# Performance work log

Hardware: AMD Instinct MI355X
Metric: run time of the kernel (lower is better)

The kernel has to match this reference:

```python
import jax, jax.numpy as jnp
import numpy as np

N_NODES = 100000
N_EDGES = 1200000
D_IN = 64
D_OUT = 64


def setup_inputs() -> dict:
    key = jax.random.key(0)
    ks = jax.random.split(key, 8)
    feat = jax.random.normal(ks[0], (N_NODES, D_IN), dtype=jnp.float32)
    src = jax.random.randint(ks[1], (N_EDGES,), 0, N_NODES, dtype=jnp.int32)
    dst = jax.random.randint(ks[2], (N_EDGES,), 0, N_NODES, dtype=jnp.int32)
    edge_weight = jax.random.uniform(ks[3], (N_EDGES, 1), dtype=jnp.float32)
    edge_mask = jax.random.uniform(ks[4], (N_EDGES, 1), dtype=jnp.float32)
    W_self = jax.random.normal(ks[5], (D_OUT, D_IN), dtype=jnp.float32) * (1.0 / np.sqrt(D_IN))
    b_self = jnp.zeros((D_OUT,), dtype=jnp.float32)
    W_neigh = jax.random.normal(ks[6], (D_OUT, D_IN), dtype=jnp.float32) * (1.0 / np.sqrt(D_IN))
    b_neigh = jnp.zeros((D_OUT,), dtype=jnp.float32)
    return {"feat": feat, "src": src, "dst": dst, "edge_weight": edge_weight,
            "edge_mask": edge_mask, "W_self": W_self, "b_self": b_self,
            "W_neigh": W_neigh, "b_neigh": b_neigh}


def reference(feat, src, dst, edge_weight, edge_mask, W_self, b_self, W_neigh, b_neigh):
    # message: gather src feats, scale by per-edge weight and mask  -> [E, D_IN]
    msg = feat[src] * edge_weight * edge_mask
    # mean scatter-reduce over incoming edges per dst node
    neigh_sum = jax.ops.segment_sum(msg, dst, num_segments=N_NODES)  # [N, D_IN]
    deg = jax.ops.segment_sum(jnp.ones((msg.shape[0],), dtype=feat.dtype), dst,
                              num_segments=N_NODES)  # [N]
    h_neigh = neigh_sum / jnp.maximum(deg, 1.0)[:, None]  # zero-degree nodes -> 0 (DGL mean semantics)
    # dual linear fuse
    rst = (feat @ W_self.T + b_self) + (h_neigh @ W_neigh.T + b_neigh)
    return rst
```

## Files before the change

### kernel.cpp

```cpp
#include <hip/hip_runtime.h>

#define NB_MAX   1568
#define CAP      1024
#define BT_EDGES 4096
#define BT_TPB   512
#define EPE      8

typedef __attribute__((ext_vector_type(4))) float floatx4;
typedef __attribute__((ext_vector_type(2))) float floatx2;
typedef __attribute__((ext_vector_type(8))) short bf16x8;

__device__ __forceinline__ unsigned short f32_to_bf16(float f) {
  unsigned u = __float_as_uint(f);
  u = (u + 0x7fffu + ((u >> 16) & 1u)) >> 16;
  return (unsigned short)u;
}
__device__ __forceinline__ unsigned pack2(float a, float b) {
  return (unsigned)f32_to_bf16(a) | ((unsigned)f32_to_bf16(b) << 16);
}
__device__ __forceinline__ bf16x8 zero_bf16x8() {
  bf16x8 v;
#pragma unroll
  for (int i = 0; i < 8; ++i) v[i] = 0;
  return v;
}

#if __has_builtin(__builtin_amdgcn_cvt_pk_fp8_f32)
__device__ __forceinline__ unsigned pack_fp8x4(float a, float b, float c, float d) {
  unsigned v = (unsigned)__builtin_amdgcn_cvt_pk_fp8_f32(a, b, 0, false);
  v = (unsigned)__builtin_amdgcn_cvt_pk_fp8_f32(c, d, (int)v, true);
  return v;
}
#else
__device__ __forceinline__ unsigned sw_f32_fp8(float f) {
  unsigned u = __float_as_uint(f);
  unsigned s = (u >> 24) & 0x80u;
  unsigned au = u & 0x7fffffffu;
  if (au > 0x43E00000u) au = 0x43E00000u;
  au += 0x7FFFFu + ((au >> 20) & 1u);
  int e = (int)(au >> 23) - 120;
  if (e <= 0) return s;
  return s | ((unsigned)e << 3) | ((au >> 20) & 7u);
}
__device__ __forceinline__ unsigned pack_fp8x4(float a, float b, float c, float d) {
  return sw_f32_fp8(a) | (sw_f32_fp8(b) << 8) | (sw_f32_fp8(c) << 16) |
         (sw_f32_fp8(d) << 24);
}
#endif

#if __has_builtin(__builtin_amdgcn_cvt_pk_f32_fp8)
__device__ __forceinline__ void dec4(float* acc, unsigned w32, float wt) {
  floatx2 f0 = __builtin_amdgcn_cvt_pk_f32_fp8((int)w32, false);
  floatx2 f1 = __builtin_amdgcn_cvt_pk_f32_fp8((int)w32, true);
  acc[0] += wt * f0.x; acc[1] += wt * f0.y;
  acc[2] += wt * f1.x; acc[3] += wt * f1.y;
}
#else
__device__ __forceinline__ float sw_fp8_f32(unsigned b) {
  unsigned s = (b & 0x80u) << 24;
  unsigned e = (b >> 3) & 0xFu;
  unsigned m = b & 7u;
  float fn = __uint_as_float(s | ((e + 120u) << 23) | (m << 20));
  float fd = (float)(int)m * 0.001953125f;
  fd = (b & 0x80u) ? -fd : fd;
  return e ? fn : fd;
}
__device__ __forceinline__ void dec4(float* acc, unsigned w32, float wt) {
  acc[0] += wt * sw_fp8_f32(w32 & 0xFF);
  acc[1] += wt * sw_fp8_f32((w32 >> 8) & 0xFF);
  acc[2] += wt * sw_fp8_f32((w32 >> 16) & 0xFF);
  acc[3] += wt * sw_fp8_f32(w32 >> 24);
}
#endif

__global__ __launch_bounds__(BT_TPB) void k_build(
    const float* __restrict__ feat, const int* __restrict__ src,
    const int* __restrict__ dst, const float* __restrict__ ew,
    const float* __restrict__ em, const float* __restrict__ Ws,
    const float* __restrict__ Wn, int* __restrict__ gCursor,
    unsigned* __restrict__ recs, unsigned short* __restrict__ featb,
    unsigned char* __restrict__ featq, unsigned short* __restrict__ Wb,
    int E, int nChunks, int nB) {
  __shared__ unsigned stage[BT_EDGES];
  __shared__ int A[NB_MAX];
  __shared__ int B[NB_MAX];
  __shared__ int waveSums[8];

  const int t = threadIdx.x;
  const int lane = t & 63;
  const int wvid = t >> 6;
  const int e0 = blockIdx.x * BT_EDGES;
  const int eEnd = min(e0 + BT_EDGES, E);
  const int nLocal = eEnd - e0;

  for (int i = t; i < NB_MAX; i += BT_TPB) B[i] = 0;
  __syncthreads();

  int dreg[EPE];
#pragma unroll
  for (int k = 0; k < EPE; ++k) {
    int i = e0 + k * BT_TPB + t;
    dreg[k] = -1;
    if (i < eEnd) {
      int d = dst[i];
      dreg[k] = d;
      atomicAdd(&B[d >> 6], 1);
    }
  }
  __syncthreads();

  {
    const int EPT = 4;
    int b0 = t * EPT;
    int v[EPT];
    int sum = 0;
#pragma unroll
    for (int j = 0; j < EPT; ++j) {
      v[j] = (b0 + j < nB) ? B[b0 + j] : 0;
      sum += v[j];
    }
    int x = sum;
#pragma unroll
    for (int d = 1; d < 64; d <<= 1) {
      int y = __shfl_up(x, d, 64);
      if (lane >= d) x += y;
    }
    if (lane == 63) waveSums[wvid] = x;
    __syncthreads();
    int wprefix = 0;
    for (int i = 0; i < wvid; ++i) wprefix += waveSums[i];
    int run = wprefix + x - sum;
#pragma unroll
    for (int j = 0; j < EPT; ++j) {
      if (b0 + j < nB) A[b0 + j] = run;
      run += v[j];
    }
  }
  __syncthreads();

  for (int i = t; i < nB; i += BT_TPB) {
    int c = B[i];
    int l = A[i];
    int g = c ? atomicAdd(&gCursor[i], c) : 0;
    A[i] = i * CAP + g - l;
    B[i] = l;
  }
  __syncthreads();

#pragma unroll
  for (int k = 0; k < EPE; ++k) {
    int i = e0 + k * BT_TPB + t;
    if (i < eEnd) {
      int d = dreg[k];
      int r = atomicAdd(&B[d >> 6], 1);
      float w = ew[i] * em[i];
      int wq = (int)(w * 511.0f + 0.5f);
      if (wq > 511) wq = 511;
      stage[r] = (unsigned)src[i] | ((unsigned)(d & 63) << 17) |
                 ((unsigned)wq << 23);
    }
  }
  __syncthreads();

  for (int i = t; i < nLocal; i += BT_TPB) {
    int lo = 0, hi = nB;
    while (lo < hi) {
      int mid = (lo + hi) >> 1;
      if (B[mid] > i) hi = mid; else lo = mid + 1;
    }
    int pos = A[lo] + i;
    if (pos < (lo + 1) * CAP)
      recs[pos] = stage[i];
  }

  for (int c = blockIdx.x * BT_TPB + t; c < nChunks; c += gridDim.x * BT_TPB) {
    const float4* fp = reinterpret_cast<const float4*>(feat) + (size_t)c * 2;
    float4 a = fp[0], b = fp[1];
    uint4 o;
    o.x = pack2(a.x, a.y);
    o.y = pack2(a.z, a.w);
    o.z = pack2(b.x, b.y);
    o.w = pack2(b.z, b.w);
    reinterpret_cast<uint4*>(featb)[c] = o;
    uint2 q8;
    q8.x = pack_fp8x4(a.x, a.y, a.z, a.w);
    q8.y = pack_fp8x4(b.x, b.y, b.z, b.w);
    reinterpret_cast<uint2*>(featq)[c] = q8;
  }

  if (blockIdx.x == 0) {
    for (int i = t; i < 1024; i += BT_TPB) {
      int j = i >> 4, c4 = i & 15;
      float4 w4 = reinterpret_cast<const float4*>(Ws)[i];
      float4 n4 = reinterpret_cast<const float4*>(Wn)[i];
      *reinterpret_cast<uint2*>(&Wb[j * 128 + c4 * 4]) =
          make_uint2(pack2(w4.x, w4.y), pack2(w4.z, w4.w));
      *reinterpret_cast<uint2*>(&Wb[j * 128 + 64 + c4 * 4]) =
          make_uint2(pack2(n4.x, n4.y), pack2(n4.z, n4.w));
    }
  }
}

__global__ __launch_bounds__(256) void sage_gather_gemm(
    const unsigned short* __restrict__ featb,
    const unsigned char* __restrict__ featq,
    const unsigned short* __restrict__ Wb, const int* __restrict__ gCursor,
    const unsigned* __restrict__ recs, const float* __restrict__ bs,
    const float* __restrict__ bn, float* __restrict__ out, int N) {
  __shared__ unsigned short An[64][72];
  __shared__ unsigned rawL[CAP];
  __shared__ unsigned srtL[CAP];
  __shared__ int cntS[64], offS[64], curS[64];

  const int t = threadIdx.x;
  const int b = blockIdx.x;
  const int n0 = b * 64;
  const int base = b * CAP;
  const int cb = min(gCursor[b], CAP);

  for (int i = t; i < cb; i += 256) rawL[i] = recs[base + i];
  if (t < 64) cntS[t] = 0;
  __syncthreads();

  for (int i = t; i < cb; i += 256)
    atomicAdd(&cntS[(rawL[i] >> 17) & 63], 1);
  __syncthreads();

  if (t < 64) {
    int c = cntS[t];
    int x = c;
#pragma unroll
    for (int d = 1; d < 64; d <<= 1) {
      int y = __shfl_up(x, d, 64);
      if (t >= d) x += y;
    }
    offS[t] = x - c;
    curS[t] = x - c;
  }
  __syncthreads();

  for (int i = t; i < cb; i += 256) {
    unsigned r = rawL[i];
    int p = atomicAdd(&curS[(r >> 17) & 63], 1);
    srtL[p] = r;
  }
  __syncthreads();

  {
    int nl = t >> 2, q = t & 3;
    int deg = cntS[nl], off = offS[nl];
    float acc[16];
#pragma unroll
    for (int i = 0; i < 16; ++i) acc[i] = 0.f;
    const uint4* fq = reinterpret_cast<const uint4*>(featq);

    uint4 uC, uN;
    float wC = 0.f, wN = 0.f;
    if (deg > 0) {
      unsigned r0 = srtL[off];
      uC = fq[(size_t)(r0 & 0x1FFFF) * 4 + q];
      wC = (float)(r0 >> 23) * (1.0f / 511.0f);
    }
    if (deg > 1) {
      unsigned r1 = srtL[off + 1];
      uN = fq[(size_t)(r1 & 0x1FFFF) * 4 + q];
      wN = (float)(r1 >> 23) * (1.0f / 511.0f);
    }
    for (int j = 0; j < deg; ++j) {
      uint4 u = uC;
      float w = wC;
      uC = uN; wC = wN;
      if (j + 2 < deg) {
        unsigned rn = srtL[off + j + 2];
        uN = fq[(size_t)(rn & 0x1FFFF) * 4 + q];
        wN = (float)(rn >> 23) * (1.0f / 511.0f);
      }
      dec4(acc + 0, u.x, w);
      dec4(acc + 4, u.y, w);
      dec4(acc + 8, u.z, w);
      dec4(acc + 12, u.w, w);
    }
    float inv = 1.0f / fmaxf((float)deg, 1.0f);
    uint4 o0, o1;
    o0.x = pack2(acc[0] * inv, acc[1] * inv);
    o0.y = pack2(acc[2] * inv, acc[3] * inv);
    o0.z = pack2(acc[4] * inv, acc[5] * inv);
    o0.w = pack2(acc[6] * inv, acc[7] * inv);
    o1.x = pack2(acc[8] * inv, acc[9] * inv);
    o1.y = pack2(acc[10] * inv, acc[11] * inv);
    o1.z = pack2(acc[12] * inv, acc[13] * inv);
    o1.w = pack2(acc[14] * inv, acc[15] * inv);
    *reinterpret_cast<uint4*>(&An[nl][q * 16]) = o0;
    *reinterpret_cast<uint4*>(&An[nl][q * 16 + 8]) = o1;
  }
  __syncthreads();

  const int wv = t >> 6;
  const int ln = t & 63;
  const int col = ln & 15;
  const int quad = ln >> 4;
  const int gn = n0 + wv * 16 + col;

  floatx4 acc4[4];
#pragma unroll
  for (int jt = 0; jt < 4; ++jt) {
    float bb = bs[jt * 16 + col] + bn[jt * 16 + col];
    acc4[jt] = (floatx4){bb, bb, bb, bb};
  }

#pragma unroll
  for (int kk = 0; kk < 4; ++kk) {
    bf16x8 af;
    if (kk < 2) {
      if (gn < N) {
        af = *reinterpret_cast<const bf16x8*>(featb + (size_t)gn * 64 + kk * 32 + quad * 8);
      } else {
        af = zero_bf16x8();
      }
    } else {
      af = *reinterpret_cast<const bf16x8*>(&An[wv * 16 + col][(kk - 2) * 32 + quad * 8]);
    }
#pragma unroll
    for (int jt = 0; jt < 4; ++jt) {
      bf16x8 bf = *reinterpret_cast<const bf16x8*>(
          Wb + (jt * 16 + col) * 128 + kk * 32 + quad * 8);
      acc4[jt] = __builtin_amdgcn_mfma_f32_16x16x32_bf16(af, bf, acc4[jt], 0, 0, 0);
    }
  }

#pragma unroll
  for (int jt = 0; jt < 4; ++jt) {
#pragma unroll
    for (int r = 0; r < 4; ++r) {
      int m = quad * 4 + r;
      int g = n0 + wv * 16 + m;
      if (g < N) out[(size_t)g * 64 + jt * 16 + col] = acc4[jt][r];
    }
  }
}

extern "C" void kernel_launch(void* const* d_in, const int* in_sizes, int n_in,
                              void* d_out, int out_size, void* d_ws, size_t ws_size,
                              hipStream_t stream) {
  const float* feat = (const float*)d_in[0];
  const int*   src  = (const int*)d_in[1];
  const int*   dst  = (const int*)d_in[2];
  const float* ew   = (const float*)d_in[3];
  const float* em   = (const float*)d_in[4];
  const float* Ws   = (const float*)d_in[5];
  const float* bs   = (const float*)d_in[6];
  const float* Wn   = (const float*)d_in[7];
  const float* bn   = (const float*)d_in[8];
  float* out = (float*)d_out;

  const int N = in_sizes[0] / 64;
  const int E = in_sizes[1];
  const int nB = (N + 63) / 64;

  unsigned short* featb = (unsigned short*)d_ws;
  unsigned char*  featq = (unsigned char*)(featb + (size_t)N * 64);
  unsigned short* Wb    = (unsigned short*)(featq + (size_t)N * 64);
  unsigned* recs   = (unsigned*)(Wb + 64 * 128);
  int*      gCursor = (int*)(recs + (size_t)NB_MAX * CAP);

  hipMemsetAsync(gCursor, 0, NB_MAX * sizeof(int), stream);

  int nChunks = N * 8;
  int gB = (E + BT_EDGES - 1) / BT_EDGES;

  k_build<<<gB, BT_TPB, 0, stream>>>(feat, src, dst, ew, em, Ws, Wn,
                                     gCursor, recs, featb, featq, Wb,
                                     E, nChunks, nB);
  sage_gather_gemm<<<nB, 256, 0, stream>>>(featb, featq, Wb, gCursor, recs,
                                           bs, bn, out, N);
}
```

Measured before the change: 163.8 us.

## Split per-node edge gather across two thread groups with 512-thread blocks

Doubles the gather/GEMM block to 512 threads. Each destination node's incoming edges are now split by parity between two 4-thread groups, and the partial sums are combined through a new shared-memory buffer before bf16 packing. The MFMA stage is split so that each of 8 waves computes half the output columns. This aims to shorten the serial per-node gather chain and raise memory-level parallelism, at the cost of more shared memory (an extra 16KB), an extra barrier, and possibly lower occupancy.

```diff
diff --git a/kernel.cpp b/kernel.cpp
--- a/kernel.cpp
+++ b/kernel.cpp
@@ -201,7 +201,7 @@
   }
 }
 
-__global__ __launch_bounds__(256) void sage_gather_gemm(
+__global__ __launch_bounds__(512) void sage_gather_gemm(
     const unsigned short* __restrict__ featb,
     const unsigned char* __restrict__ featq,
     const unsigned short* __restrict__ Wb, const int* __restrict__ gCursor,
@@ -210,6 +210,7 @@
   __shared__ unsigned short An[64][72];
   __shared__ unsigned rawL[CAP];
   __shared__ unsigned srtL[CAP];
+  __shared__ float pf[64][64];
   __shared__ int cntS[64], offS[64], curS[64];
 
   const int t = threadIdx.x;
@@ -218,11 +219,11 @@
   const int base = b * CAP;
   const int cb = min(gCursor[b], CAP);
 
-  for (int i = t; i < cb; i += 256) rawL[i] = recs[base + i];
+  for (int i = t; i < cb; i += 512) rawL[i] = recs[base + i];
   if (t < 64) cntS[t] = 0;
   __syncthreads();
 
-  for (int i = t; i < cb; i += 256)
+  for (int i = t; i < cb; i += 512)
     atomicAdd(&cntS[(rawL[i] >> 17) & 63], 1);
   __syncthreads();
 
@@ -239,7 +240,7 @@
   }
   __syncthreads();
 
-  for (int i = t; i < cb; i += 256) {
+  for (int i = t; i < cb; i += 512) {
     unsigned r = rawL[i];
     int p = atomicAdd(&curS[(r >> 17) & 63], 1);
     srtL[p] = r;
@@ -247,8 +248,11 @@
   __syncthreads();
 
   {
-    int nl = t >> 2, q = t & 3;
-    int deg = cntS[nl], off = offS[nl];
+    const int nl = t >> 3;
+    const int g  = (t >> 2) & 1;
+    const int q  = t & 3;
+    const int deg = cntS[nl], off = offS[nl];
+    const int myN = (deg - g + 1) >> 1;
     float acc[16];
 #pragma unroll
     for (int i = 0; i < 16; ++i) acc[i] = 0.f;
@@ -256,22 +260,22 @@
 
     uint4 uC, uN;
     float wC = 0.f, wN = 0.f;
-    if (deg > 0) {
-      unsigned r0 = srtL[off];
+    if (myN > 0) {
+      unsigned r0 = srtL[off + g];
       uC = fq[(size_t)(r0 & 0x1FFFF) * 4 + q];
       wC = (float)(r0 >> 23) * (1.0f / 511.0f);
     }
-    if (deg > 1) {
-      unsigned r1 = srtL[off + 1];
+    if (myN > 1) {
+      unsigned r1 = srtL[off + g + 2];
       uN = fq[(size_t)(r1 & 0x1FFFF) * 4 + q];
       wN = (float)(r1 >> 23) * (1.0f / 511.0f);
     }
-    for (int j = 0; j < deg; ++j) {
+    for (int m = 0; m < myN; ++m) {
       uint4 u = uC;
       float w = wC;
       uC = uN; wC = wN;
-      if (j + 2 < deg) {
-        unsigned rn = srtL[off + j + 2];
+      if (m + 2 < myN) {
+        unsigned rn = srtL[off + g + 2 * (m + 2)];
         uN = fq[(size_t)(rn & 0x1FFFF) * 4 + q];
         wN = (float)(rn >> 23) * (1.0f / 511.0f);
       }
@@ -280,32 +284,45 @@
       dec4(acc + 8, u.z, w);
       dec4(acc + 12, u.w, w);
     }
-    float inv = 1.0f / fmaxf((float)deg, 1.0f);
-    uint4 o0, o1;
-    o0.x = pack2(acc[0] * inv, acc[1] * inv);
-    o0.y = pack2(acc[2] * inv, acc[3] * inv);
-    o0.z = pack2(acc[4] * inv, acc[5] * inv);
-    o0.w = pack2(acc[6] * inv, acc[7] * inv);
-    o1.x = pack2(acc[8] * inv, acc[9] * inv);
-    o1.y = pack2(acc[10] * inv, acc[11] * inv);
-    o1.z = pack2(acc[12] * inv, acc[13] * inv);
-    o1.w = pack2(acc[14] * inv, acc[15] * inv);
-    *reinterpret_cast<uint4*>(&An[nl][q * 16]) = o0;
-    *reinterpret_cast<uint4*>(&An[nl][q * 16 + 8]) = o1;
-  }
-  __syncthreads();
-
-  const int wv = t >> 6;
+
+    if (g == 1) {
+#pragma unroll
+      for (int i = 0; i < 16; ++i) pf[nl][q * 16 + i] = acc[i];
+    }
+    __syncthreads();
+    if (g == 0) {
+      float inv = 1.0f / fmaxf((float)deg, 1.0f);
+#pragma unroll
+      for (int i = 0; i < 16; ++i) acc[i] = (acc[i] + pf[nl][q * 16 + i]) * inv;
+      uint4 o0, o1;
+      o0.x = pack2(acc[0], acc[1]);
+      o0.y = pack2(acc[2], acc[3]);
+      o0.z = pack2(acc[4], acc[5]);
+      o0.w = pack2(acc[6], acc[7]);
+      o1.x = pack2(acc[8], acc[9]);
+      o1.y = pack2(acc[10], acc[11]);
+      o1.z = pack2(acc[12], acc[13]);
+      o1.w = pack2(acc[14], acc[15]);
+      *reinterpret_cast<uint4*>(&An[nl][q * 16]) = o0;
+      *reinterpret_cast<uint4*>(&An[nl][q * 16 + 8]) = o1;
+    }
+  }
+  __syncthreads();
+
+  const int wv8 = t >> 6;
+  const int nt = wv8 & 3;
+  const int jh = wv8 >> 2;
   const int ln = t & 63;
   const int col = ln & 15;
   const int quad = ln >> 4;
-  const int gn = n0 + wv * 16 + col;
-
-  floatx4 acc4[4];
-#pragma unroll
-  for (int jt = 0; jt < 4; ++jt) {
+  const int gn = n0 + nt * 16 + col;
+
+  floatx4 acc4[2];
+#pragma unroll
+  for (int jj = 0; jj < 2; ++jj) {
+    int jt = jh * 2 + jj;
     float bb = bs[jt * 16 + col] + bn[jt * 16 + col];
-    acc4[jt] = (floatx4){bb, bb, bb, bb};
+    acc4[jj] = (floatx4){bb, bb, bb, bb};
   }
 
 #pragma unroll
@@ -318,23 +335,25 @@
         af = zero_bf16x8();
       }
     } else {
-      af = *reinterpret_cast<const bf16x8*>(&An[wv * 16 + col][(kk - 2) * 32 + quad * 8]);
-    }
-#pragma unroll
-    for (int jt = 0; jt < 4; ++jt) {
+      af = *reinterpret_cast<const bf16x8*>(&An[nt * 16 + col][(kk - 2) * 32 + quad * 8]);
+    }
+#pragma unroll
+    for (int jj = 0; jj < 2; ++jj) {
+      int jt = jh * 2 + jj;
       bf16x8 bf = *reinterpret_cast<const bf16x8*>(
           Wb + (jt * 16 + col) * 128 + kk * 32 + quad * 8);
-      acc4[jt] = __builtin_amdgcn_mfma_f32_16x16x32_bf16(af, bf, acc4[jt], 0, 0, 0);
-    }
-  }
-
-#pragma unroll
-  for (int jt = 0; jt < 4; ++jt) {
+      acc4[jj] = __builtin_amdgcn_mfma_f32_16x16x32_bf16(af, bf, acc4[jj], 0, 0, 0);
+    }
+  }
+
+#pragma unroll
+  for (int jj = 0; jj < 2; ++jj) {
+    int jt = jh * 2 + jj;
 #pragma unroll
     for (int r = 0; r < 4; ++r) {
       int m = quad * 4 + r;
-      int g = n0 + wv * 16 + m;
-      if (g < N) out[(size_t)g * 64 + jt * 16 + col] = acc4[jt][r];
+      int g2 = n0 + nt * 16 + m;
+      if (g2 < N) out[(size_t)g2 * 64 + jt * 16 + col] = acc4[jj][r];
     }
   }
 }
@@ -371,6 +390,6 @@
   k_build<<<gB, BT_TPB, 0, stream>>>(feat, src, dst, ew, em, Ws, Wn,
                                      gCursor, recs, featb, featq, Wb,
                                      E, nChunks, nB);
-  sage_gather_gemm<<<nB, 256, 0, stream>>>(featb, featq, Wb, gCursor, recs,
+  sage_gather_gemm<<<nB, 512, 0, stream>>>(featb, featq, Wb, gCursor, recs,
                                            bs, bn, out, N);
 }
```

After: 162.0 us. Within noise of the previous version (-1.1%).
